# Kernel optimization log

Measured on AMD Instinct MI355X. Metric: run time of the kernel, lower is better.

## Reference

```python
import jax, jax.numpy as jnp
import numpy as np

NUM_NODES = 32768  # B*N = 16*2048
NUM_REL = 10
NUM_BASES = 4
D = 256
E = 524288


def _rgcn_layer(x, src, dst, rel, basis, comp, root, bias):
    """Basis-decomposed relational GCN layer with per-relation mean aggregation.
    x: [N, Din], basis: [NB, Din, Dout], comp: [R, NB], root: [Din, Dout], bias: [Dout].
    """
    n = x.shape[0]
    # project all nodes through each basis once: [N, NB, Dout]
    xb = jnp.einsum('ni,bio->nbo', x, basis)
    coeff = comp[rel]  # [E, NB] per-edge basis coefficients
    # mean normalization per (destination node, relation) pair
    seg = rel * n + dst  # combined segment id, [E]
    cnt = jax.ops.segment_sum(jnp.ones(rel.shape[0], x.dtype), seg,
                              num_segments=NUM_REL * n)
    inv = jnp.where(cnt > 0, 1.0 / cnt, 0.0)[seg]  # [E]
    # per-edge message: sum_b coeff[e,b] * xb[src_e, b, :] (loop over small NB)
    msg = jnp.zeros((rel.shape[0], basis.shape[2]), x.dtype)
    for b in range(basis.shape[0]):
        msg = msg + coeff[:, b:b + 1] * xb[src, b]
    msg = msg * inv[:, None]
    agg = jax.ops.segment_sum(msg, dst, num_segments=n)  # [N, Dout]
    return agg + x @ root + bias


def setup_inputs() -> dict:
    key = jax.random.key(0)
    ks = jax.random.split(key, 16)
    p = lambda k, shp: (jax.random.normal(k, shp, jnp.float32) * 0.05)
    inp = {
        'x': jax.random.normal(ks[0], (16, 2048, D), jnp.float32),
        't': jax.random.randint(ks[1], (16,), 0, 1000),
        'obj_cond': jax.random.randint(ks[2], (16, 2048), 0, 160),
        'edge_cond': jax.random.randint(ks[3], (2, E), 0, NUM_NODES),
        'relation_cond': jax.random.randint(ks[4], (E,), 0, NUM_REL),
        # layer 0: 256 -> 256 (hidden)
        'basis0': p(ks[5], (NUM_BASES, D, D)),
        'comp0': p(ks[6], (NUM_REL, NUM_BASES)),
        'root0': p(ks[7], (D, D)),
        'bias0': p(ks[8], (D,)),
        # layer 1: 256 -> 256 (output)
        'basis1': p(ks[9], (NUM_BASES, D, D)),
        'comp1': p(ks[10], (NUM_REL, NUM_BASES)),
        'root1': p(ks[11], (D, D)),
        'bias1': p(ks[12], (D,)),
    }
    return inp


def reference(x, t, obj_cond, edge_cond, relation_cond,
              basis0, comp0, root0, bias0, basis1, comp1, root1, bias1):
    B, N, Dm = x.shape
    h = x.reshape(B * N, Dm)
    src, dst = edge_cond[0], edge_cond[1]
    h = _rgcn_layer(h, src, dst, relation_cond, basis0, comp0, root0, bias0)
    h = jax.nn.relu(h)  # hidden-layer activation (dropout disabled at eval)
    h = _rgcn_layer(h, src, dst, relation_cond, basis1, comp1, root1, bias1)
    return h.reshape(B, N, Dm)
```

## Files before the change

kernel.cpp:

```cpp
#include <hip/hip_runtime.h>
#include <stdint.h>

#define NNODES 32768
#define NREL 10
#define NBASES 4
#define DIM 256
#define NEDGE 524288
#define KW 1280
#define KBASE 1024

#define HB 2048
#define CB 8192
#define WB 80

typedef __attribute__((ext_vector_type(8))) short bf16x8;
typedef __attribute__((ext_vector_type(4))) float f32x4;
typedef __attribute__((ext_vector_type(2))) float f32x2;

__device__ __forceinline__ float bf2f(unsigned short u){
  union { unsigned int i; float f; } v; v.i = ((unsigned int)u) << 16; return v.f;
}
__device__ __forceinline__ float asf(unsigned int u){
  union { unsigned int i; float f; } v; v.i = u; return v.f;
}
__device__ __forceinline__ unsigned short f2bf(float f){
  union { float f; unsigned int i; } v; v.f = f;
  unsigned int x = v.i;
  unsigned int r = (x + 0x7FFFu + ((x >> 16) & 1u)) >> 16;
  return (unsigned short)r;
}
__device__ __forceinline__ void gll16(const void* g, void* l){
  __builtin_amdgcn_global_load_lds((const __attribute__((address_space(1))) void*)g,
                                   (__attribute__((address_space(3))) void*)l, 16, 0, 0);
}

__global__ __launch_bounds__(256) void mega_prep(
    const int* __restrict__ ec, const int* __restrict__ rel,
    int* __restrict__ cnt_rd,
    const float* __restrict__ x, unsigned short* __restrict__ Xh,
    const float* __restrict__ basis0, const float* __restrict__ root0,
    unsigned short* __restrict__ Wt0,
    const float* __restrict__ basis1, const float* __restrict__ root1,
    unsigned short* __restrict__ Wt1)
{
  __shared__ float tile[64][65];
  int bid = blockIdx.x;
  int t = threadIdx.x;
  if (bid < HB){
    int e = bid * 256 + t;
    int d = ec[NEDGE + e];
    int r = rel[e];
    atomicAdd(&cnt_rd[(r << 15) + d], 1);
  } else if (bid < HB + CB){
    int i = (bid - HB) * 256 + t;
    float4 v = ((const float4*)x)[i];
    ushort4 o; o.x = f2bf(v.x); o.y = f2bf(v.y); o.z = f2bf(v.z); o.w = f2bf(v.w);
    ((ushort4*)Xh)[i] = o;
  } else {
    int b = bid - HB - CB;
    int layer = b / WB; b %= WB;
    const float* basis = layer ? basis1 : basis0;
    const float* root  = layer ? root1  : root0;
    unsigned short* Wt = layer ? Wt1    : Wt0;
    int k0 = (b % 20) * 64;
    int n0 = (b / 20) * 64;
    int tn = t & 63, tk = t >> 6;
#pragma unroll
    for (int i = 0; i < 64; i += 4){
      int k = k0 + tk + i;
      float v = (k < KBASE) ? basis[(size_t)k * 256 + n0 + tn]
                            : root[(size_t)(k - KBASE) * 256 + n0 + tn];
      tile[tk + i][tn] = v;
    }
    __syncthreads();
#pragma unroll
    for (int i = 0; i < 64; i += 4){
      int n = n0 + tk + i;
      Wt[(size_t)n * KW + k0 + tn] = f2bf(tile[tn][tk + i]);
    }
  }
}

__global__ __launch_bounds__(1024) void scan1(const int* __restrict__ cnt_rd,
                                              int* __restrict__ offs, int* __restrict__ blksum)
{
  __shared__ int wsum[16];
  int tid = threadIdx.x; int gid = blockIdx.x * 1024 + tid;
  int lane = tid & 63, wv = tid >> 6;
  int v = 0;
#pragma unroll
  for (int r = 0; r < NREL; r++) v += cnt_rd[(r << 15) + gid];
  int incl = v;
#pragma unroll
  for (int o = 1; o < 64; o <<= 1){
    int t = __shfl_up(incl, o);
    if (lane >= o) incl += t;
  }
  if (lane == 63) wsum[wv] = incl;
  __syncthreads();
  if (wv == 0){
    int s = (lane < 16) ? wsum[lane] : 0;
#pragma unroll
    for (int o = 1; o < 16; o <<= 1){
      int t = __shfl_up(s, o);
      if (lane >= o) s += t;
    }
    if (lane < 16) wsum[lane] = s;
  }
  __syncthreads();
  int base = wv ? wsum[wv - 1] : 0;
  offs[gid] = base + incl - v;
  if (tid == 1023) blksum[blockIdx.x] = base + incl;
}
__global__ __launch_bounds__(1024) void scan3b(int* __restrict__ offs, const int* __restrict__ blksum)
{
  __shared__ int pre;
  int bid = blockIdx.x;
  if (threadIdx.x < 64){
    int v = ((int)threadIdx.x < bid && threadIdx.x < 32) ? blksum[threadIdx.x] : 0;
#pragma unroll
    for (int o = 1; o < 64; o <<= 1) v += __shfl_xor(v, o);
    if (threadIdx.x == 0) pre = v;
  }
  __syncthreads();
  int gid = bid * 1024 + threadIdx.x;
  offs[gid] += pre;
}

__global__ void scatter_kernel(const int* __restrict__ ec, const int* __restrict__ rel,
                               int* __restrict__ offs,
                               unsigned int* __restrict__ meta)
{
  int e = blockIdx.x * 256 + threadIdx.x;
  int s = ec[e];
  int d = ec[NEDGE + e];
  int r = rel[e];
  int p = atomicAdd(&offs[d], 1);
  meta[p] = ((unsigned int)s << 4) | (unsigned int)r;
}

__global__ __launch_bounds__(256) void agg8(
    const unsigned short* __restrict__ Xin,
    const int* __restrict__ offs,
    const unsigned int* __restrict__ meta,
    const float* __restrict__ comp,
    const int* __restrict__ cnt_rd,
    unsigned short* __restrict__ z)
{
  __shared__ __attribute__((aligned(16))) float wtab[4][40];
  int t = threadIdx.x;
  int wv = t >> 6, lane = t & 63;
  int d = blockIdx.x * 4 + wv;
  if (lane < 40){
    int r = lane >> 2, b = lane & 3;
    int cnt = cnt_rd[(r << 15) + d];
    wtab[wv][lane] = (cnt > 0) ? comp[r * NBASES + b] / (float)cnt : 0.0f;
  }
  __syncthreads();

  const float4* wt4 = (const float4*)&wtab[wv][0];
  const char* Xb = (const char*)Xin;
  unsigned colb = (unsigned)(lane * 8);

  f32x2 acc[NBASES][2];
#pragma unroll
  for (int b = 0; b < NBASES; b++){ acc[b][0] = (f32x2){0.f,0.f}; acc[b][1] = (f32x2){0.f,0.f}; }

  int e1 = offs[d];
  int e0 = (d == 0) ? 0 : offs[d - 1];
  int e = e0;

  for (; e + 7 < e1; e += 8){
    unsigned int m[8];
#pragma unroll
    for (int i = 0; i < 8; i++) m[i] = meta[e + i];
    uint2 v[8];
#pragma unroll
    for (int i = 0; i < 8; i++){
      unsigned off = ((m[i] & 0xFFFFFFF0u) << 5) + colb;
      v[i] = *(const uint2*)(Xb + off);
    }
#pragma unroll
    for (int i = 0; i < 8; i++){
      float4 w = wt4[m[i] & 15u];
      f32x2 f01, f23;
      f01.x = asf(v[i].x << 16); f01.y = asf(v[i].x & 0xffff0000u);
      f23.x = asf(v[i].y << 16); f23.y = asf(v[i].y & 0xffff0000u);
      acc[0][0] += (f32x2){w.x, w.x} * f01;  acc[0][1] += (f32x2){w.x, w.x} * f23;
      acc[1][0] += (f32x2){w.y, w.y} * f01;  acc[1][1] += (f32x2){w.y, w.y} * f23;
      acc[2][0] += (f32x2){w.z, w.z} * f01;  acc[2][1] += (f32x2){w.z, w.z} * f23;
      acc[3][0] += (f32x2){w.w, w.w} * f01;  acc[3][1] += (f32x2){w.w, w.w} * f23;
    }
  }

  for (; e < e1; e += 4){
    unsigned int m[4];
    float4 w[4];
#pragma unroll
    for (int i = 0; i < 4; i++){
      int ei = e + i;
      bool ok = ei < e1;
      m[i] = meta[ok ? ei : e1 - 1];
      float4 ww = wt4[m[i] & 15u];
      if (!ok){ ww.x = 0.f; ww.y = 0.f; ww.z = 0.f; ww.w = 0.f; }
      w[i] = ww;
    }
    uint2 v[4];
#pragma unroll
    for (int i = 0; i < 4; i++){
      unsigned off = ((m[i] & 0xFFFFFFF0u) << 5) + colb;
      v[i] = *(const uint2*)(Xb + off);
    }
#pragma unroll
    for (int i = 0; i < 4; i++){
      f32x2 f01, f23;
      f01.x = asf(v[i].x << 16); f01.y = asf(v[i].x & 0xffff0000u);
      f23.x = asf(v[i].y << 16); f23.y = asf(v[i].y & 0xffff0000u);
      acc[0][0] += (f32x2){w[i].x, w[i].x} * f01;  acc[0][1] += (f32x2){w[i].x, w[i].x} * f23;
      acc[1][0] += (f32x2){w[i].y, w[i].y} * f01;  acc[1][1] += (f32x2){w[i].y, w[i].y} * f23;
      acc[2][0] += (f32x2){w[i].z, w[i].z} * f01;  acc[2][1] += (f32x2){w[i].z, w[i].z} * f23;
      acc[3][0] += (f32x2){w[i].w, w[i].w} * f01;  acc[3][1] += (f32x2){w[i].w, w[i].w} * f23;
    }
  }

#pragma unroll
  for (int b = 0; b < NBASES; b++){
    ushort4 o;
    o.x = f2bf(acc[b][0].x); o.y = f2bf(acc[b][0].y);
    o.z = f2bf(acc[b][1].x); o.w = f2bf(acc[b][1].y);
    *(ushort4*)(z + (size_t)d * KBASE + b * 256 + lane * 4) = o;
  }
}

__global__ __launch_bounds__(256) void gemm9(
    const unsigned short* __restrict__ A0,
    const unsigned short* __restrict__ A1,
    const unsigned short* __restrict__ Wt,
    const float* __restrict__ bias,
    unsigned short* __restrict__ outh,
    float* __restrict__ outf,
    int mode)
{
  __shared__ __attribute__((aligned(16))) short As[128 * 32];
  __shared__ __attribute__((aligned(16))) short Bs[128 * 32];
  int tid  = threadIdx.x;
  int bid  = blockIdx.x;
  int m0   = (bid >> 1) * 128;
  int n0   = (bid & 1) * 128;
  int lane = tid & 63;
  int w    = tid >> 6;
  int wm   = w >> 1, wn = w & 1;
  int lq = lane >> 4, lr = lane & 15;

  f32x4 zero = {0.f, 0.f, 0.f, 0.f};
  f32x4 acc[4][4];
#pragma unroll
  for (int i = 0; i < 4; i++)
#pragma unroll
    for (int j = 0; j < 4; j++) acc[i][j] = zero;

  int g1   = tid + 256;
  int ar0  = tid >> 2, ak0 = ((tid & 3) - (tid >> 3)) & 3;
  int ar1  = g1 >> 2,  ak1 = ((g1 & 3) - (g1 >> 3)) & 3;

  for (int k0 = 0; k0 < KW; k0 += 32){
    __syncthreads();
    {
      const unsigned short *ga0, *ga1;
      if (k0 < KBASE){
        ga0 = A0 + (size_t)(m0 + ar0) * KBASE + k0 + ak0 * 8;
        ga1 = A0 + (size_t)(m0 + ar1) * KBASE + k0 + ak1 * 8;
      } else {
        ga0 = A1 + (size_t)(m0 + ar0) * 256 + (k0 - KBASE) + ak0 * 8;
        ga1 = A1 + (size_t)(m0 + ar1) * 256 + (k0 - KBASE) + ak1 * 8;
      }
      gll16(ga0, As + tid * 8);
      gll16(ga1, As + g1 * 8);
      gll16(Wt + (size_t)(n0 + ar0) * KW + k0 + ak0 * 8, Bs + tid * 8);
      gll16(Wt + (size_t)(n0 + ar1) * KW + k0 + ak1 * 8, Bs + g1 * 8);
    }
    __syncthreads();

    bf16x8 af[4], bfr[4];
#pragma unroll
    for (int i = 0; i < 4; i++){
      int row = wm * 64 + i * 16 + lr;
      af[i] = *(const bf16x8*)(As + row * 32 + (((lq + (row >> 1)) & 3) * 8));
    }
#pragma unroll
    for (int j = 0; j < 4; j++){
      int row = wn * 64 + j * 16 + lr;
      bfr[j] = *(const bf16x8*)(Bs + row * 32 + (((lq + (row >> 1)) & 3) * 8));
    }
#pragma unroll
    for (int i = 0; i < 4; i++)
#pragma unroll
      for (int j = 0; j < 4; j++)
        acc[i][j] = __builtin_amdgcn_mfma_f32_16x16x32_bf16(af[i], bfr[j], acc[i][j], 0, 0, 0);
  }

#pragma unroll
  for (int i = 0; i < 4; i++)
#pragma unroll
    for (int j = 0; j < 4; j++)
#pragma unroll
      for (int r = 0; r < 4; r++){
        int gm = m0 + wm * 64 + i * 16 + lq * 4 + r;
        int gn = n0 + wn * 64 + j * 16 + lr;
        float v = acc[i][j][r] + bias[gn];
        size_t idx = (size_t)gm * 256 + gn;
        if (mode == 1) outh[idx] = f2bf(fmaxf(v, 0.f));
        else           outf[idx] = v;
      }
}

extern "C" void kernel_launch(void* const* d_in, const int* in_sizes, int n_in,
                              void* d_out, int out_size, void* d_ws, size_t ws_size,
                              hipStream_t stream)
{
  const float* x      = (const float*)d_in[0];
  const int*   ec     = (const int*)d_in[3];
  const int*   rel    = (const int*)d_in[4];
  const float* basis0 = (const float*)d_in[5];
  const float* comp0  = (const float*)d_in[6];
  const float* root0  = (const float*)d_in[7];
  const float* bias0  = (const float*)d_in[8];
  const float* basis1 = (const float*)d_in[9];
  const float* comp1  = (const float*)d_in[10];
  const float* root1  = (const float*)d_in[11];
  const float* bias1  = (const float*)d_in[12];

  char* p = (char*)d_ws;
  unsigned short* z   = (unsigned short*)p; p += (size_t)NNODES * KBASE * 2;
  unsigned short* Xh  = (unsigned short*)p; p += (size_t)NNODES * DIM * 2;
  unsigned short* h   = (unsigned short*)p; p += (size_t)NNODES * DIM * 2;
  unsigned short* Wt0 = (unsigned short*)p; p += (size_t)256 * KW * 2;
  unsigned short* Wt1 = (unsigned short*)p; p += (size_t)256 * KW * 2;
  unsigned int* meta  = (unsigned int*)p;   p += (size_t)NEDGE * 4;
  int* cnt_rd  = (int*)p;   p += (size_t)NREL * NNODES * 4;
  int* offs    = (int*)p;   p += (size_t)(NNODES + 1) * 4;
  int* blksum  = (int*)p;   p += 1024;

  hipMemsetAsync(cnt_rd, 0, (size_t)NREL * NNODES * 4, stream);

  mega_prep<<<HB + CB + 2 * WB, 256, 0, stream>>>(
      ec, rel, cnt_rd, x, Xh, basis0, root0, Wt0, basis1, root1, Wt1);

  scan1<<<NNODES / 1024, 1024, 0, stream>>>(cnt_rd, offs, blksum);
  scan3b<<<NNODES / 1024, 1024, 0, stream>>>(offs, blksum);
  scatter_kernel<<<NEDGE / 256, 256, 0, stream>>>(ec, rel, offs, meta);

  agg8<<<NNODES / 4, 256, 0, stream>>>(Xh, offs, meta, comp0, cnt_rd, z);
  gemm9<<<(NNODES / 128) * 2, 256, 0, stream>>>(z, Xh, Wt0, bias0, h, nullptr, 1);

  agg8<<<NNODES / 4, 256, 0, stream>>>(h, offs, meta, comp1, cnt_rd, z);
  gemm9<<<(NNODES / 128) * 2, 256, 0, stream>>>(z, h, Wt1, bias1, nullptr, (float*)d_out, 2);
}
```

Before: 322.3 us.

## Fuse CSR build (count, scan, scatter) into one cooperative kernel

Replaces the memset, histogram part of mega_prep, two scan kernels and the scatter kernel with a single cooperative-launch kernel that uses grid-wide syncs between phases. The aim is to remove several kernel launches and their inter-kernel gaps. In exchange it adds grid.sync barriers and a serial single-block scan of 512 block sums, and the edge histogram no longer overlaps with the bf16 conversion work.

```diff
diff --git a/kernel.cpp b/kernel.cpp
--- a/kernel.cpp
+++ b/kernel.cpp
@@ -1,5 +1,8 @@
 #include <hip/hip_runtime.h>
+#include <hip/hip_cooperative_groups.h>
 #include <stdint.h>
+
+namespace cg = cooperative_groups;
 
 #define NNODES 32768
 #define NREL 10
@@ -9,9 +12,11 @@
 #define KW 1280
 #define KBASE 1024
 
-#define HB 2048
 #define CB 8192
 #define WB 80
+
+#define CSRB 512
+#define CSRT 256
 
 typedef __attribute__((ext_vector_type(8))) short bf16x8;
 typedef __attribute__((ext_vector_type(4))) float f32x4;
@@ -35,8 +40,6 @@
 }
 
 __global__ __launch_bounds__(256) void mega_prep(
-    const int* __restrict__ ec, const int* __restrict__ rel,
-    int* __restrict__ cnt_rd,
     const float* __restrict__ x, unsigned short* __restrict__ Xh,
     const float* __restrict__ basis0, const float* __restrict__ root0,
     unsigned short* __restrict__ Wt0,
@@ -46,18 +49,13 @@
   __shared__ float tile[64][65];
   int bid = blockIdx.x;
   int t = threadIdx.x;
-  if (bid < HB){
-    int e = bid * 256 + t;
-    int d = ec[NEDGE + e];
-    int r = rel[e];
-    atomicAdd(&cnt_rd[(r << 15) + d], 1);
-  } else if (bid < HB + CB){
-    int i = (bid - HB) * 256 + t;
+  if (bid < CB){
+    int i = bid * 256 + t;
     float4 v = ((const float4*)x)[i];
     ushort4 o; o.x = f2bf(v.x); o.y = f2bf(v.y); o.z = f2bf(v.z); o.w = f2bf(v.w);
     ((ushort4*)Xh)[i] = o;
   } else {
-    int b = bid - HB - CB;
+    int b = bid - CB;
     int layer = b / WB; b %= WB;
     const float* basis = layer ? basis1 : basis0;
     const float* root  = layer ? root1  : root0;
@@ -81,62 +79,84 @@
   }
 }
 
-__global__ __launch_bounds__(1024) void scan1(const int* __restrict__ cnt_rd,
-                                              int* __restrict__ offs, int* __restrict__ blksum)
-{
-  __shared__ int wsum[16];
-  int tid = threadIdx.x; int gid = blockIdx.x * 1024 + tid;
-  int lane = tid & 63, wv = tid >> 6;
-  int v = 0;
-#pragma unroll
-  for (int r = 0; r < NREL; r++) v += cnt_rd[(r << 15) + gid];
-  int incl = v;
-#pragma unroll
-  for (int o = 1; o < 64; o <<= 1){
-    int t = __shfl_up(incl, o);
-    if (lane >= o) incl += t;
-  }
-  if (lane == 63) wsum[wv] = incl;
-  __syncthreads();
-  if (wv == 0){
-    int s = (lane < 16) ? wsum[lane] : 0;
-#pragma unroll
-    for (int o = 1; o < 16; o <<= 1){
-      int t = __shfl_up(s, o);
-      if (lane >= o) s += t;
-    }
-    if (lane < 16) wsum[lane] = s;
-  }
-  __syncthreads();
-  int base = wv ? wsum[wv - 1] : 0;
-  offs[gid] = base + incl - v;
-  if (tid == 1023) blksum[blockIdx.x] = base + incl;
-}
-__global__ __launch_bounds__(1024) void scan3b(int* __restrict__ offs, const int* __restrict__ blksum)
-{
-  __shared__ int pre;
-  int bid = blockIdx.x;
-  if (threadIdx.x < 64){
-    int v = ((int)threadIdx.x < bid && threadIdx.x < 32) ? blksum[threadIdx.x] : 0;
-#pragma unroll
-    for (int o = 1; o < 64; o <<= 1) v += __shfl_xor(v, o);
-    if (threadIdx.x == 0) pre = v;
-  }
-  __syncthreads();
-  int gid = bid * 1024 + threadIdx.x;
-  offs[gid] += pre;
-}
-
-__global__ void scatter_kernel(const int* __restrict__ ec, const int* __restrict__ rel,
-                               int* __restrict__ offs,
-                               unsigned int* __restrict__ meta)
-{
-  int e = blockIdx.x * 256 + threadIdx.x;
-  int s = ec[e];
-  int d = ec[NEDGE + e];
-  int r = rel[e];
-  int p = atomicAdd(&offs[d], 1);
-  meta[p] = ((unsigned int)s << 4) | (unsigned int)r;
+__global__ __launch_bounds__(CSRT) void csr_build(
+    const int* __restrict__ ec, const int* __restrict__ rel,
+    int* __restrict__ cnt_rd, int* __restrict__ offs,
+    int* __restrict__ blksum, unsigned int* __restrict__ meta)
+{
+  cg::grid_group grid = cg::this_grid();
+  int tid = threadIdx.x, bid = blockIdx.x;
+  int gtid = bid * CSRT + tid;
+
+  for (int i = gtid; i < NREL * NNODES; i += CSRB * CSRT) cnt_rd[i] = 0;
+  grid.sync();
+
+  for (int e = gtid; e < NEDGE; e += CSRB * CSRT){
+    int d = ec[NEDGE + e];
+    int r = rel[e];
+    atomicAdd(&cnt_rd[(r << 15) + d], 1);
+  }
+  grid.sync();
+
+  {
+    int nb = bid * 64;
+    if (tid < 64){
+      int d = nb + tid;
+      int deg = 0;
+#pragma unroll
+      for (int r = 0; r < NREL; r++) deg += cnt_rd[(r << 15) + d];
+      int incl = deg;
+#pragma unroll
+      for (int o = 1; o < 64; o <<= 1){
+        int t2 = __shfl_up(incl, o);
+        if (tid >= o) incl += t2;
+      }
+      offs[d] = incl - deg;
+      if (tid == 63) blksum[bid] = incl;
+    }
+  }
+  grid.sync();
+
+  if (bid == 0){
+    __shared__ int wtot[4];
+    __shared__ int carry;
+    if (tid == 0) carry = 0;
+    __syncthreads();
+    int lane = tid & 63, wv = tid >> 6;
+    for (int c = 0; c < 2; c++){
+      int v = blksum[c * 256 + tid];
+      int incl = v;
+#pragma unroll
+      for (int o = 1; o < 64; o <<= 1){
+        int t2 = __shfl_up(incl, o);
+        if (lane >= o) incl += t2;
+      }
+      if (lane == 63) wtot[wv] = incl;
+      __syncthreads();
+      int base = carry;
+      for (int wj = 0; wj < 4; wj++) if (wj < wv) base += wtot[wj];
+      int excl = base + incl - v;
+      blksum[c * 256 + tid] = excl;
+      __syncthreads();
+      if (tid == 255) carry = excl + v;
+      __syncthreads();
+    }
+  }
+  grid.sync();
+
+  if (tid < 64){
+    int d = bid * 64 + tid;
+    offs[d] += blksum[bid];
+  }
+  grid.sync();
+
+  for (int e = gtid; e < NEDGE; e += CSRB * CSRT){
+    int s = ec[e];
+    int d = ec[NEDGE + e];
+    int r = rel[e];
+    int p = atomicAdd(&offs[d], 1);
+    meta[p] = ((unsigned int)s << 4) | (unsigned int)r;
+  }
 }
 
 __global__ __launch_bounds__(256) void agg8(
@@ -339,16 +359,17 @@
   unsigned int* meta  = (unsigned int*)p;   p += (size_t)NEDGE * 4;
   int* cnt_rd  = (int*)p;   p += (size_t)NREL * NNODES * 4;
   int* offs    = (int*)p;   p += (size_t)(NNODES + 1) * 4;
-  int* blksum  = (int*)p;   p += 1024;
-
-  hipMemsetAsync(cnt_rd, 0, (size_t)NREL * NNODES * 4, stream);
-
-  mega_prep<<<HB + CB + 2 * WB, 256, 0, stream>>>(
-      ec, rel, cnt_rd, x, Xh, basis0, root0, Wt0, basis1, root1, Wt1);
-
-  scan1<<<NNODES / 1024, 1024, 0, stream>>>(cnt_rd, offs, blksum);
-  scan3b<<<NNODES / 1024, 1024, 0, stream>>>(offs, blksum);
-  scatter_kernel<<<NEDGE / 256, 256, 0, stream>>>(ec, rel, offs, meta);
+  int* blksum  = (int*)p;   p += 1024 * 4;
+
+  {
+    void* args[] = { (void*)&ec, (void*)&rel, (void*)&cnt_rd, (void*)&offs,
+                     (void*)&blksum, (void*)&meta };
+    hipLaunchCooperativeKernel((const void*)csr_build, dim3(CSRB), dim3(CSRT),
+                               args, 0, stream);
+  }
+
+  mega_prep<<<CB + 2 * WB, 256, 0, stream>>>(
+      x, Xh, basis0, root0, Wt0, basis1, root1, Wt1);
 
   agg8<<<NNODES / 4, 256, 0, stream>>>(Xh, offs, meta, comp0, cnt_rd, z);
   gemm9<<<(NNODES / 128) * 2, 256, 0, stream>>>(z, Xh, Wt0, bias0, h, nullptr, 1);
```

After: 597.5 us. 85.3% more time.
